# Kernel tuning notes

Measured on AMD Instinct MI355X. Metric: run time of the kernel, lower is better.

Reference implementation:

```python
import jax, jax.numpy as jnp
import numpy as np

B, N, S = 4, 8192, 2048
C1, C2 = 128, 256
CIN = C1 + C2  # 384
H1, H2 = 256, 256
BN_EPS = 1e-5


def setup_inputs() -> dict:
    key = jax.random.key(0)
    ks = jax.random.split(key, 12)
    inp = {
        "xyz1": jax.random.normal(ks[0], (B, N, 3), jnp.float32),
        "xyz2": jax.random.normal(ks[1], (B, S, 3), jnp.float32),
        "points1": jax.random.normal(ks[2], (B, C1, N), jnp.float32),
        "points2": jax.random.normal(ks[3], (B, C2, S), jnp.float32),
        # Conv1d(k=1) weights are [out, in]; BN affine params per channel
        "W1": jax.random.normal(ks[4], (H1, CIN), jnp.float32) * (1.0 / np.sqrt(CIN)),
        "b1": jnp.zeros((H1,), jnp.float32),
        "gamma1": jnp.ones((H1,), jnp.float32),
        "beta1": jnp.zeros((H1,), jnp.float32),
        "W2": jax.random.normal(ks[5], (H2, H1), jnp.float32) * (1.0 / np.sqrt(H1)),
        "b2": jnp.zeros((H2,), jnp.float32),
        "gamma2": jnp.ones((H2,), jnp.float32),
        "beta2": jnp.zeros((H2,), jnp.float32),
    }
    return inp


def _square_distance(src, dst):
    # src [B,N,3], dst [B,S,3] -> [B,N,S]
    d = -2.0 * jnp.einsum("bnc,bsc->bns", src, dst)
    d = d + jnp.sum(src * src, -1)[:, :, None]
    d = d + jnp.sum(dst * dst, -1)[:, None, :]
    return jnp.maximum(d, 0.0)


def _bn_relu(x, gamma, beta):
    # x [B,C,N]; BatchNorm1d in training mode: batch stats over (B, N), biased var
    mean = jnp.mean(x, axis=(0, 2), keepdims=True)
    var = jnp.mean((x - mean) ** 2, axis=(0, 2), keepdims=True)
    xhat = (x - mean) * jax.lax.rsqrt(var + BN_EPS)
    return jax.nn.relu(xhat * gamma[None, :, None] + beta[None, :, None])


def reference(xyz1, xyz2, points1, points2, W1, b1, gamma1, beta1, W2, b2, gamma2, beta2):
    dists = _square_distance(xyz1, xyz2)            # [B,N,S]
    neg_d, idx = jax.lax.top_k(-dists, 3)           # 3 smallest distances
    d3 = -neg_d                                     # [B,N,3]
    recip = 1.0 / (d3 + 1e-8)
    weight = recip / jnp.sum(recip, axis=2, keepdims=True)  # [B,N,3]
    pts2 = jnp.transpose(points2, (0, 2, 1))        # [B,S,C2]
    gathered = jax.vmap(lambda p, i: p[i])(pts2, idx)  # [B,N,3,C2]
    interp = jnp.einsum("bnkc,bnk->bcn", gathered, weight)  # [B,C2,N]
    new_pts = jnp.concatenate([points1, interp], axis=1)    # [B,CIN,N]
    x = jnp.einsum("oc,bcn->bon", W1, new_pts) + b1[None, :, None]
    x = _bn_relu(x, gamma1, beta1)
    x = jnp.einsum("oc,bcn->bon", W2, x) + b2[None, :, None]
    x = _bn_relu(x, gamma2, beta2)
    return x
```

## Files before the change

kernel.cpp:

```cpp
#include <hip/hip_runtime.h>

#define B_   4
#define N_   8192
#define S_   2048
#define C1_  128
#define C2_  256
#define CIN_ 384
#define H_   256

typedef short short8 __attribute__((ext_vector_type(8)));
typedef unsigned short ushort8 __attribute__((ext_vector_type(8)));
typedef float f32x4 __attribute__((ext_vector_type(4)));

__device__ __forceinline__ unsigned short f2bf(float x) {
  unsigned u = __float_as_uint(x);
  unsigned r = (u + 0x7fffu + ((u >> 16) & 1u)) >> 16;
  return (unsigned short)r;
}
__device__ __forceinline__ float bf2f(unsigned short h) {
  return __uint_as_float(((unsigned)h) << 16);
}
__device__ __forceinline__ void async16(const void* g, void* l) {
  __builtin_amdgcn_global_load_lds(
      (const __attribute__((address_space(1))) void*)g,
      (__attribute__((address_space(3))) void*)l, 16, 0, 0);
}

__global__ __launch_bounds__(256) void convw_kernel(const float* __restrict__ W1,
                                                    const float* __restrict__ W2,
                                                    unsigned short* __restrict__ W1b,
                                                    unsigned short* __restrict__ W2b) {
  int id = blockIdx.x * 256 + threadIdx.x;
  if (id < 98304) W1b[id] = f2bf(W1[id]);
  else            W2b[id - 98304] = f2bf(W2[id - 98304]);
}

__global__ __launch_bounds__(512) void knn_kernel(const float* __restrict__ xyz1,
                                                  const float* __restrict__ xyz2,
                                                  int* __restrict__ idx,
                                                  float* __restrict__ wgt) {
  __shared__ float4 t4[S_];
  __shared__ float kd[64][25];
  __shared__ int   ki[64][25];
  const int b  = blockIdx.x >> 7;
  const int n0 = (blockIdx.x & 127) << 6;
  const int tid = threadIdx.x;

  for (int i = tid; i < S_; i += 512) {
    float x = xyz2[(b * S_ + i) * 3 + 0];
    float y = xyz2[(b * S_ + i) * 3 + 1];
    float z = xyz2[(b * S_ + i) * 3 + 2];
    t4[i] = make_float4(-2.f * x, -2.f * y, -2.f * z,
                        fmaf(x, x, fmaf(y, y, z * z)));
  }
  __syncthreads();

  const int w = tid >> 6;
  const int ln = tid & 63;
  const int n = n0 + ln;
  const float px = xyz1[(b * N_ + n) * 3 + 0];
  const float py = xyz1[(b * N_ + n) * 3 + 1];
  const float pz = xyz1[(b * N_ + n) * 3 + 2];
  const float h = fmaf(px, px, fmaf(py, py, pz * pz));

  float d0 = 1e30f, d1 = 1e30f, d2 = 1e30f;
  int j0 = 0, j1 = 0, j2 = 0;
  const int jg0 = w * 256;
  const float4* tp = t4 + jg0;
#pragma unroll 4
  for (int j = 0; j < 256; ++j) {
    float4 t = tp[j];
    float d = fmaf(px, t.x, fmaf(py, t.y, fmaf(pz, t.z, t.w))) + h;
    d = fmaxf(d, 0.f);
    const int jj = jg0 + j;
    bool c0 = d < d0, c1 = d < d1, c2 = d < d2;
    float nd2 = c1 ? d1 : (c2 ? d : d2);
    int   nj2 = c1 ? j1 : (c2 ? jj : j2);
    float nd1 = c0 ? d0 : (c1 ? d : d1);
    int   nj1 = c0 ? j0 : (c1 ? jj : j1);
    d0 = c0 ? d : d0;
    j0 = c0 ? jj : j0;
    d1 = nd1; j1 = nj1;
    d2 = nd2; j2 = nj2;
  }
  kd[ln][w * 3 + 0] = d0; ki[ln][w * 3 + 0] = j0;
  kd[ln][w * 3 + 1] = d1; ki[ln][w * 3 + 1] = j1;
  kd[ln][w * 3 + 2] = d2; ki[ln][w * 3 + 2] = j2;
  __syncthreads();

  if (tid < 64) {
    float m0 = kd[tid][0], m1 = kd[tid][1], m2 = kd[tid][2];
    int   i0 = ki[tid][0], i1 = ki[tid][1], i2 = ki[tid][2];
#pragma unroll
    for (int s = 3; s < 24; ++s) {
      float d = kd[tid][s];
      int  jj = ki[tid][s];
      bool c0 = d < m0, c1 = d < m1, c2 = d < m2;
      float nd2 = c1 ? m1 : (c2 ? d : m2);
      int   nj2 = c1 ? i1 : (c2 ? jj : i2);
      float nd1 = c0 ? m0 : (c1 ? d : m1);
      int   nj1 = c0 ? i0 : (c1 ? jj : i1);
      m0 = c0 ? d : m0;
      i0 = c0 ? jj : i0;
      m1 = nd1; i1 = nj1;
      m2 = nd2; i2 = nj2;
    }
    float r0 = 1.f / (m0 + 1e-8f);
    float r1 = 1.f / (m1 + 1e-8f);
    float r2 = 1.f / (m2 + 1e-8f);
    float rs = 1.f / (r0 + r1 + r2);
    int base = (b * N_ + n0 + tid) * 3;
    idx[base + 0] = i0;
    idx[base + 1] = i1;
    idx[base + 2] = i2;
    wgt[base + 0] = r0 * rs;
    wgt[base + 1] = r1 * rs;
    wgt[base + 2] = r2 * rs;
  }
}

__global__ __launch_bounds__(256) void interp_kernel(const float* __restrict__ p2,
                                                     const int* __restrict__ idx,
                                                     const float* __restrict__ wgt,
                                                     float* __restrict__ Xint) {
  __shared__ float rows[4][S_];
  const int b = blockIdx.x >> 6;
  const int cg = blockIdx.x & 63;
  const int tid = threadIdx.x;
  for (int i = tid; i < 4 * S_; i += 256)
    rows[i >> 11][i & (S_ - 1)] =
        p2[((size_t)b * C2_ + cg * 4 + (i >> 11)) * S_ + (i & (S_ - 1))];
  __syncthreads();
  for (int n = tid; n < N_; n += 256) {
    int base = (b * N_ + n) * 3;
    int i0 = idx[base], i1 = idx[base + 1], i2 = idx[base + 2];
    float w0 = wgt[base], w1 = wgt[base + 1], w2 = wgt[base + 2];
#pragma unroll
    for (int cc = 0; cc < 4; ++cc) {
      float v = w0 * rows[cc][i0] + w1 * rows[cc][i1] + w2 * rows[cc][i2];
      Xint[((size_t)b * C2_ + cg * 4 + cc) * N_ + n] = v;
    }
  }
}

__global__ __launch_bounds__(256) void transpose_bf16_kernel(
    const float* __restrict__ p1, const float* __restrict__ Xint,
    unsigned short* __restrict__ Xt) {
  __shared__ float tile[64 * 65];
  const int b = blockIdx.z;
  const int ct = blockIdx.y;
  const int n0 = blockIdx.x * 64;
  const int c0 = ct * 64;
  const int tid = threadIdx.x;
  const float* src = (ct < 2) ? (p1 + ((size_t)b * C1_ + c0) * N_)
                              : (Xint + ((size_t)b * C2_ + (c0 - C1_)) * N_);
  const int c_l = tid >> 2, nch = (tid & 3) * 16;
  const float* sp = src + (size_t)c_l * N_ + n0 + nch;
#pragma unroll
  for (int i = 0; i < 4; ++i)
    *(float4*)&tile[c_l * 65 + nch + i * 4] = *(const float4*)(sp + i * 4);
  __syncthreads();
  const int n_l = tid >> 2, cch = (tid & 3) * 16;
  unsigned short pk[16];
#pragma unroll
  for (int i = 0; i < 16; ++i) pk[i] = f2bf(tile[(cch + i) * 65 + n_l]);
  unsigned short* dst = Xt + (size_t)(b * N_ + n0 + n_l) * CIN_ + c0 + cch;
  *(uint4*)dst = *(uint4*)pk;
  *(uint4*)(dst + 8) = *(uint4*)(pk + 8);
}

template <int K, bool FUSE>
__global__ __launch_bounds__(256, 2) void gemm_mfma_kernel(
    const unsigned short* __restrict__ Wb,
    const unsigned short* __restrict__ Bmat,
    const float* __restrict__ bias,
    const float* __restrict__ bnscale, const float* __restrict__ bnshift,
    float* __restrict__ OutF, unsigned short* __restrict__ OutB,
    float* __restrict__ Psum, float* __restrict__ Psq) {
  __shared__ __align__(16) short Als[128 * 32];
  __shared__ __align__(16) short Bls[128 * 32];
  const int tid = threadIdx.x;
  const int lane = tid & 63;
  const int col = lane & 15, quad = lane >> 4;
  const int wid = tid >> 6;
  const int wr = wid >> 1, wc = wid & 1;
  const int nBase = blockIdx.x * 128;
  const int oBase = blockIdx.y * 128;
  const int b = blockIdx.z;

  f32x4 acc[4][4];
#pragma unroll
  for (int i = 0; i < 4; ++i)
#pragma unroll
    for (int j = 0; j < 4; ++j) acc[i][j] = (f32x4){0.f, 0.f, 0.f, 0.f};

  const int f0 = tid * 16;
  const int m0 = f0 >> 6;
  const int kb0 = f0 & 63;
  const char* Abase = (const char*)Wb;
  const char* Bbase = (const char*)Bmat;
  char* AldsW = (char*)Als + (tid & ~63) * 16;
  char* BldsW = (char*)Bls + (tid & ~63) * 16;

  for (int k0 = 0; k0 < K; k0 += 32) {
    __syncthreads();
    async16(Abase + ((size_t)(oBase + m0) * K + k0) * 2 + kb0, AldsW);
    async16(Abase + ((size_t)(oBase + m0 + 64) * K + k0) * 2 + kb0, AldsW + 4096);
    if (!FUSE) {
      async16(Bbase + ((size_t)(b * N_ + nBase + m0) * K + k0) * 2 + kb0, BldsW);
      async16(Bbase + ((size_t)(b * N_ + nBase + m0 + 64) * K + k0) * 2 + kb0,
              BldsW + 4096);
    } else {
#pragma unroll
      for (int r = 0; r < 2; ++r) {
        const int f = f0 + r * 4096;
        const int n = f >> 6;
        const int kb = f & 63;
        const int ke = k0 + (kb >> 1);
        ushort8 h = *(const ushort8*)(Bbase +
            ((size_t)(b * N_ + nBase + n) * K + k0) * 2 + kb);
        float4 s0 = *(const float4*)(bnscale + ke);
        float4 s1 = *(const float4*)(bnscale + ke + 4);
        float4 t0 = *(const float4*)(bnshift + ke);
        float4 t1 = *(const float4*)(bnshift + ke + 4);
        float sc[8] = {s0.x, s0.y, s0.z, s0.w, s1.x, s1.y, s1.z, s1.w};
        float sh[8] = {t0.x, t0.y, t0.z, t0.w, t1.x, t1.y, t1.z, t1.w};
        unsigned short pk[8];
#pragma unroll
        for (int e = 0; e < 8; ++e)
          pk[e] = f2bf(fmaxf(fmaf(bf2f(h[e]), sc[e], sh[e]), 0.f));
        *(uint4*)((char*)Bls + f) = *(uint4*)pk;
      }
    }
    __syncthreads();
    short8 af[4], bfr[4];
#pragma unroll
    for (int i = 0; i < 4; ++i)
      af[i] = *(const short8*)(Als + (wr * 64 + i * 16 + col) * 32 + quad * 8);
#pragma unroll
    for (int j = 0; j < 4; ++j)
      bfr[j] = *(const short8*)(Bls + (wc * 64 + j * 16 + col) * 32 + quad * 8);
#pragma unroll
    for (int i = 0; i < 4; ++i)
#pragma unroll
      for (int j = 0; j < 4; ++j)
        acc[i][j] = __builtin_amdgcn_mfma_f32_16x16x32_bf16(af[i], bfr[j],
                                                            acc[i][j], 0, 0, 0);
  }

  float s_acc[4][4], q_acc[4][4];
#pragma unroll
  for (int i = 0; i < 4; ++i) {
    const int oloc = wr * 64 + i * 16 + quad * 4;
    float4 bb = *(const float4*)(bias + oBase + oloc);
    float s[4] = {0.f, 0.f, 0.f, 0.f}, q[4] = {0.f, 0.f, 0.f, 0.f};
#pragma unroll
    for (int j = 0; j < 4; ++j) {
      const int n = nBase + wc * 64 + j * 16 + col;
      float v0 = acc[i][j][0] + bb.x;
      float v1 = acc[i][j][1] + bb.y;
      float v2 = acc[i][j][2] + bb.z;
      float v3 = acc[i][j][3] + bb.w;
      if (!FUSE) {
        unsigned short pk[4] = {f2bf(v0), f2bf(v1), f2bf(v2), f2bf(v3)};
        *(uint2*)(OutB + (size_t)(b * N_ + n) * H_ + oBase + oloc) = *(uint2*)pk;
      } else {
        float* op = OutF + ((size_t)b * H_ + oBase + oloc) * N_ + n;
        op[0] = v0; op[N_] = v1; op[2 * N_] = v2; op[3 * N_] = v3;
      }
      s[0] += v0; q[0] = fmaf(v0, v0, q[0]);
      s[1] += v1; q[1] = fmaf(v1, v1, q[1]);
      s[2] += v2; q[2] = fmaf(v2, v2, q[2]);
      s[3] += v3; q[3] = fmaf(v3, v3, q[3]);
    }
#pragma unroll
    for (int reg = 0; reg < 4; ++reg) {
      float ss = s[reg], qq = q[reg];
#pragma unroll
      for (int m = 1; m < 16; m <<= 1) {
        ss += __shfl_xor(ss, m);
        qq += __shfl_xor(qq, m);
      }
      s_acc[i][reg] = ss;
      q_acc[i][reg] = qq;
    }
  }
  __syncthreads();
  float* red = (float*)Als;
#pragma unroll
  for (int i = 0; i < 4; ++i)
#pragma unroll
    for (int reg = 0; reg < 4; ++reg)
      if (col == 0) {
        int ch = wr * 64 + i * 16 + quad * 4 + reg;
        red[wc * 256 + ch] = s_acc[i][reg];
        red[wc * 256 + 128 + ch] = q_acc[i][reg];
      }
  __syncthreads();
  {
    const int wcb = tid >> 7, ch = tid & 127;
    const int part = (blockIdx.z * 64 + blockIdx.x) * 2 + wcb;
    Psum[part * 256 + oBase + ch] = red[wcb * 256 + ch];
    Psq[part * 256 + oBase + ch]  = red[wcb * 256 + 128 + ch];
  }
}

__global__ __launch_bounds__(1024) void finalize_bn_kernel(
    const float* __restrict__ Psum, const float* __restrict__ Psq,
    const float* __restrict__ gamma, const float* __restrict__ beta,
    float* __restrict__ scale, float* __restrict__ shift) {
  __shared__ float ls[4][2][256];
  const int tid = threadIdx.x;
  const int g = tid >> 8, ch = tid & 255;
  float s = 0.f, q = 0.f;
#pragma unroll 4
  for (int p = g * 128; p < (g + 1) * 128; ++p) {
    s += Psum[p * 256 + ch];
    q += Psq[p * 256 + ch];
  }
  ls[g][0][ch] = s;
  ls[g][1][ch] = q;
  __syncthreads();
  if (tid < 256) {
    float ss = ls[0][0][ch] + ls[1][0][ch] + ls[2][0][ch] + ls[3][0][ch];
    float qq = ls[0][1][ch] + ls[1][1][ch] + ls[2][1][ch] + ls[3][1][ch];
    const float inv_n = 1.f / 32768.f;
    float mean = ss * inv_n;
    float var = qq * inv_n - mean * mean;
    float sc = gamma[ch] * rsqrtf(var + 1e-5f);
    scale[ch] = sc;
    shift[ch] = fmaf(-mean, sc, beta[ch]);
  }
}

__global__ __launch_bounds__(256) void bn_apply_kernel(float* __restrict__ io,
                                                       const float* __restrict__ scale,
                                                       const float* __restrict__ shift) {
  int id = blockIdx.x * 256 + threadIdx.x;
  int row = id >> 11;
  int o = row & 255;
  float sc = scale[o], sh = shift[o];
  float4 v = ((float4*)io)[id];
  v.x = fmaxf(fmaf(v.x, sc, sh), 0.f);
  v.y = fmaxf(fmaf(v.y, sc, sh), 0.f);
  v.z = fmaxf(fmaf(v.z, sc, sh), 0.f);
  v.w = fmaxf(fmaf(v.w, sc, sh), 0.f);
  ((float4*)io)[id] = v;
}

extern "C" void kernel_launch(void* const* d_in, const int* in_sizes, int n_in,
                              void* d_out, int out_size, void* d_ws, size_t ws_size,
                              hipStream_t stream) {
  const float* xyz1 = (const float*)d_in[0];
  const float* xyz2 = (const float*)d_in[1];
  const float* p1   = (const float*)d_in[2];
  const float* p2   = (const float*)d_in[3];
  const float* W1   = (const float*)d_in[4];
  const float* b1   = (const float*)d_in[5];
  const float* g1   = (const float*)d_in[6];
  const float* be1  = (const float*)d_in[7];
  const float* W2   = (const float*)d_in[8];
  const float* b2   = (const float*)d_in[9];
  const float* g2   = (const float*)d_in[10];
  const float* be2  = (const float*)d_in[11];
  float* out = (float*)d_out;

  float* ws = (float*)d_ws;
  float* Xint = ws;
  unsigned short* Xt  = (unsigned short*)(Xint + 8388608);
  unsigned short* Y1t = Xt + 12582912;
  unsigned short* W1b = Y1t + 8388608;
  unsigned short* W2b = W1b + 98304;
  float* wgt   = (float*)(W2b + 65536);
  int*   idxb  = (int*)(wgt + 98304);
  float* Psum1 = (float*)(idxb + 98304);
  float* Psq1  = Psum1 + 131072;
  float* Psum2 = Psq1 + 131072;
  float* Psq2  = Psum2 + 131072;
  float* scale1 = Psq2 + 131072;
  float* shift1 = scale1 + 256;
  float* scale2 = shift1 + 256;
  float* shift2 = scale2 + 256;

  convw_kernel<<<640, 256, 0, stream>>>(W1, W2, W1b, W2b);
  knn_kernel<<<512, 512, 0, stream>>>(xyz1, xyz2, idxb, wgt);
  interp_kernel<<<256, 256, 0, stream>>>(p2, idxb, wgt, Xint);
  transpose_bf16_kernel<<<dim3(128, 6, 4), 256, 0, stream>>>(p1, Xint, Xt);

  dim3 gg(64, 2, 4);
  gemm_mfma_kernel<CIN_, false><<<gg, 256, 0, stream>>>(
      W1b, Xt, b1, nullptr, nullptr, nullptr, Y1t, Psum1, Psq1);
  finalize_bn_kernel<<<1, 1024, 0, stream>>>(Psum1, Psq1, g1, be1, scale1, shift1);
  gemm_mfma_kernel<H_, true><<<gg, 256, 0, stream>>>(
      W2b, Y1t, b2, scale1, shift1, out, nullptr, Psum2, Psq2);
  finalize_bn_kernel<<<1, 1024, 0, stream>>>(Psum2, Psq2, g2, be2, scale2, shift2);
  bn_apply_kernel<<<8192, 256, 0, stream>>>(out, scale2, shift2);
}
```

Baseline: 221.8 us.

## Gather interpolation directly from transposed bf16 points2 into GEMM input

Transposes points2 once into a bf16 [B,S,C2] layout, then has each wavefront gather the three neighbour rows and write the interpolated bf16 values straight into the channel-last GEMM input. This removes the fp32 Xint intermediate and the second transpose pass over it, cutting global traffic. points1 is now transposed by a generic transpose kernel. Interpolation inputs are rounded to bf16 before weighting, which adds a little rounding error, and the gather reads scattered 512-byte rows.

```diff
diff --git a/kernel.cpp b/kernel.cpp
--- a/kernel.cpp
+++ b/kernel.cpp
@@ -33,6 +33,33 @@
   int id = blockIdx.x * 256 + threadIdx.x;
   if (id < 98304) W1b[id] = f2bf(W1[id]);
   else            W2b[id - 98304] = f2bf(W2[id - 98304]);
+}
+
+__global__ __launch_bounds__(256) void transpose_kernel(
+    const float* __restrict__ src, unsigned short* __restrict__ dst,
+    int dstStride) {
+  __shared__ float tile[64 * 65];
+  const int b = blockIdx.z;
+  const int n0 = blockIdx.x * 64;
+  const int c0 = blockIdx.y * 64;
+  const int C = gridDim.y * 64;
+  const int Nsrc = gridDim.x * 64;
+  const int tid = threadIdx.x;
+  const float* sp = src + ((size_t)b * C + c0) * Nsrc;
+  unsigned short* dp = dst + (size_t)b * Nsrc * dstStride;
+  const int c_l = tid >> 2, nch = (tid & 3) * 16;
+  const float* s = sp + (size_t)c_l * Nsrc + n0 + nch;
+#pragma unroll
+  for (int i = 0; i < 4; ++i)
+    *(float4*)&tile[c_l * 65 + nch + i * 4] = *(const float4*)(s + i * 4);
+  __syncthreads();
+  const int n_l = tid >> 2, cch = (tid & 3) * 16;
+  unsigned short pk[16];
+#pragma unroll
+  for (int i = 0; i < 16; ++i) pk[i] = f2bf(tile[(cch + i) * 65 + n_l]);
+  unsigned short* d = dp + (size_t)(n0 + n_l) * dstStride + c0 + cch;
+  *(uint4*)d = *(uint4*)pk;
+  *(uint4*)(d + 8) = *(uint4*)(pk + 8);
 }
 
 __global__ __launch_bounds__(512) void knn_kernel(const float* __restrict__ xyz1,
@@ -119,54 +146,35 @@
   }
 }
 
-__global__ __launch_bounds__(256) void interp_kernel(const float* __restrict__ p2,
-                                                     const int* __restrict__ idx,
-                                                     const float* __restrict__ wgt,
-                                                     float* __restrict__ Xint) {
-  __shared__ float rows[4][S_];
-  const int b = blockIdx.x >> 6;
-  const int cg = blockIdx.x & 63;
-  const int tid = threadIdx.x;
-  for (int i = tid; i < 4 * S_; i += 256)
-    rows[i >> 11][i & (S_ - 1)] =
-        p2[((size_t)b * C2_ + cg * 4 + (i >> 11)) * S_ + (i & (S_ - 1))];
-  __syncthreads();
-  for (int n = tid; n < N_; n += 256) {
-    int base = (b * N_ + n) * 3;
+__global__ __launch_bounds__(256) void interp_gather_kernel(
+    const unsigned short* __restrict__ p2t, const int* __restrict__ idx,
+    const float* __restrict__ wgt, unsigned short* __restrict__ Xt) {
+  const int w = threadIdx.x >> 6, lane = threadIdx.x & 63;
+  const int gbase = blockIdx.x * 128 + w * 32;
+#pragma unroll 2
+  for (int i = 0; i < 32; ++i) {
+    const int gn = gbase + i;
+    const int b = gn >> 13;
+    const int base = gn * 3;
     int i0 = idx[base], i1 = idx[base + 1], i2 = idx[base + 2];
     float w0 = wgt[base], w1 = wgt[base + 1], w2 = wgt[base + 2];
-#pragma unroll
-    for (int cc = 0; cc < 4; ++cc) {
-      float v = w0 * rows[cc][i0] + w1 * rows[cc][i1] + w2 * rows[cc][i2];
-      Xint[((size_t)b * C2_ + cg * 4 + cc) * N_ + n] = v;
+    const unsigned short* r0 = p2t + (((size_t)(b * S_ + i0)) << 8) + lane * 4;
+    const unsigned short* r1 = p2t + (((size_t)(b * S_ + i1)) << 8) + lane * 4;
+    const unsigned short* r2 = p2t + (((size_t)(b * S_ + i2)) << 8) + lane * 4;
+    uint2 a = *(const uint2*)r0;
+    uint2 c = *(const uint2*)r1;
+    uint2 e = *(const uint2*)r2;
+    const unsigned short* ap = (const unsigned short*)&a;
+    const unsigned short* cp = (const unsigned short*)&c;
+    const unsigned short* ep = (const unsigned short*)&e;
+    unsigned short pk[4];
+#pragma unroll
+    for (int k = 0; k < 4; ++k) {
+      float v = w0 * bf2f(ap[k]) + w1 * bf2f(cp[k]) + w2 * bf2f(ep[k]);
+      pk[k] = f2bf(v);
     }
-  }
-}
-
-__global__ __launch_bounds__(256) void transpose_bf16_kernel(
-    const float* __restrict__ p1, const float* __restrict__ Xint,
-    unsigned short* __restrict__ Xt) {
-  __shared__ float tile[64 * 65];
-  const int b = blockIdx.z;
-  const int ct = blockIdx.y;
-  const int n0 = blockIdx.x * 64;
-  const int c0 = ct * 64;
-  const int tid = threadIdx.x;
-  const float* src = (ct < 2) ? (p1 + ((size_t)b * C1_ + c0) * N_)
-                              : (Xint + ((size_t)b * C2_ + (c0 - C1_)) * N_);
-  const int c_l = tid >> 2, nch = (tid & 3) * 16;
-  const float* sp = src + (size_t)c_l * N_ + n0 + nch;
-#pragma unroll
-  for (int i = 0; i < 4; ++i)
-    *(float4*)&tile[c_l * 65 + nch + i * 4] = *(const float4*)(sp + i * 4);
-  __syncthreads();
-  const int n_l = tid >> 2, cch = (tid & 3) * 16;
-  unsigned short pk[16];
-#pragma unroll
-  for (int i = 0; i < 16; ++i) pk[i] = f2bf(tile[(cch + i) * 65 + n_l]);
-  unsigned short* dst = Xt + (size_t)(b * N_ + n0 + n_l) * CIN_ + c0 + cch;
-  *(uint4*)dst = *(uint4*)pk;
-  *(uint4*)(dst + 8) = *(uint4*)(pk + 8);
+    *(uint2*)(Xt + (size_t)gn * CIN_ + C1_ + lane * 4) = *(uint2*)pk;
+  }
 }
 
 template <int K, bool FUSE>
@@ -365,11 +373,11 @@
   const float* be2  = (const float*)d_in[11];
   float* out = (float*)d_out;
 
-  float* ws = (float*)d_ws;
-  float* Xint = ws;
-  unsigned short* Xt  = (unsigned short*)(Xint + 8388608);
+  unsigned short* ws = (unsigned short*)d_ws;
+  unsigned short* Xt  = ws;
   unsigned short* Y1t = Xt + 12582912;
-  unsigned short* W1b = Y1t + 8388608;
+  unsigned short* p2t = Y1t + 8388608;
+  unsigned short* W1b = p2t + 2097152;
   unsigned short* W2b = W1b + 98304;
   float* wgt   = (float*)(W2b + 65536);
   int*   idxb  = (int*)(wgt + 98304);
@@ -383,9 +391,10 @@
   float* shift2 = scale2 + 256;
 
   convw_kernel<<<640, 256, 0, stream>>>(W1, W2, W1b, W2b);
+  transpose_kernel<<<dim3(32, 4, 4), 256, 0, stream>>>(p2, p2t, C2_);
   knn_kernel<<<512, 512, 0, stream>>>(xyz1, xyz2, idxb, wgt);
-  interp_kernel<<<256, 256, 0, stream>>>(p2, idxb, wgt, Xint);
-  transpose_bf16_kernel<<<dim3(128, 6, 4), 256, 0, stream>>>(p1, Xint, Xt);
+  transpose_kernel<<<dim3(128, 2, 4), 256, 0, stream>>>(p1, Xt, CIN_);
+  interp_gather_kernel<<<256, 256, 0, stream>>>(p2t, idxb, wgt, Xt);
 
   dim3 gg(64, 2, 4);
   gemm_mfma_kernel<CIN_, false><<<gg, 256, 0, stream>>>(
```

New measurement: 220.6 us. Within noise of the previous version (-0.5%).
